# Kernel tuning notes

Measured on AMD Instinct MI355X. Metric: run time of the kernel, lower is better.

Reference implementation:

```python
import jax, jax.numpy as jnp
import numpy as np

B, SE, HD, ED, N, T = 64, 512, 1024, 512, 10000, 20
EOS_ID = 1
NEG_BIG = -1e9    # stand-in for -MAX_VAL encoder pad mask
MASK_VAL = -1e7   # logits_mask scatter value (-10000000.0 in torch)
M = HD + ED


def setup_inputs() -> dict:
    key = jax.random.key(0)
    ks = jax.random.split(key, 16)
    s = 0.02
    enc = jax.random.normal(ks[0], (B, SE, HD), jnp.float32)
    hidden = jax.random.normal(ks[1], (1, B, HD), jnp.float32)
    cell = jax.random.normal(ks[2], (1, B, HD), jnp.float32)
    text_lengths = jax.random.randint(ks[3], (B,), SE // 2, SE + 1)
    encoder_mask = jnp.arange(SE)[None, :] < text_lengths[:, None]  # [B,SE] bool
    embedding = jax.random.normal(ks[4], (N, ED), jnp.float32) * s
    # LSTM (PyTorch gate order i,f,g,o)
    w_ih = jax.random.normal(ks[5], (4 * HD, ED), jnp.float32) * s
    w_hh = jax.random.normal(ks[6], (4 * HD, HD), jnp.float32) * s
    b_ih = jnp.zeros((4 * HD,), jnp.float32)
    b_hh = jnp.zeros((4 * HD,), jnp.float32)
    # dense_net: Hd -> He
    w_q = jax.random.normal(ks[7], (HD, HD), jnp.float32) * s
    b_q = jnp.zeros((HD,), jnp.float32)
    # SelfAttentiveSum: Linear(Ed,Ed)+ReLU+Linear(Ed,1)
    w_k = jax.random.normal(ks[8], (ED, ED), jnp.float32) * s
    b_k = jnp.zeros((ED,), jnp.float32)
    w_ko = jax.random.normal(ks[9], (ED,), jnp.float32) * s
    b_ko = jnp.zeros((), jnp.float32)
    # MLP: Linear(M,M)+ReLU+Linear(M,N)
    w_m1 = jax.random.normal(ks[10], (M, M), jnp.float32) * s
    b_m1 = jnp.zeros((M,), jnp.float32)
    w_m2 = jax.random.normal(ks[11], (N, M), jnp.float32) * s
    b_m2 = jnp.zeros((N,), jnp.float32)
    return dict(encoded_hidden_embeddings=enc, hidden=hidden, cell=cell,
                text_lengths=text_lengths, encoder_mask=encoder_mask,
                embedding=embedding, w_ih=w_ih, w_hh=w_hh, b_ih=b_ih, b_hh=b_hh,
                w_q=w_q, b_q=b_q, w_k=w_k, b_k=b_k, w_ko=w_ko, b_ko=b_ko,
                w_m1=w_m1, b_m1=b_m1, w_m2=w_m2, b_m2=b_m2)


def _decode(enc, h0, c0, encoder_mask, embedding, w_ih, w_hh, b_ih, b_hh,
            w_q, b_q, w_k, b_k, w_ko, b_ko, w_m1, b_m1, w_m2, b_m2):
    pad_mask = jnp.where(encoder_mask, 0.0, NEG_BIG).astype(enc.dtype)  # [B,SE]
    sent = enc[:, 0, :]  # [B,HD] sentence representation (dropout is identity in eval)

    def step(carry, t):
        h, c, inp, logits_mask, buf = carry
        # --- LSTM cell (single step) ---
        gates = inp @ w_ih.T + b_ih + h @ w_hh.T + b_hh  # [B,4HD]
        i, f, g, o = jnp.split(gates, 4, axis=-1)
        c = jax.nn.sigmoid(f) * c + jax.nn.sigmoid(i) * jnp.tanh(g)
        h = jax.nn.sigmoid(o) * jnp.tanh(c)
        # --- attention over encoder states ---
        q = h @ w_q.T + b_q                                   # [B,HD]
        score = jnp.einsum('bsh,bh->bs', enc, q) + pad_mask    # [B,SE]
        w = jax.nn.softmax(score, axis=1)
        attn_enc = jnp.einsum('bs,bsh->bh', w, enc)            # [B,HD]
        # --- self-attentive sum over previously predicted label embeddings ---
        valid = jnp.arange(T) < jnp.maximum(t, 1)              # step 0: zeros row 0 valid
        k = jax.nn.relu(buf @ w_k.T + b_k) @ w_ko + b_ko       # [B,T]
        k = jnp.where(valid[None, :], k, NEG_BIG)
        sw = jax.nn.softmax(k, axis=1)
        attn_last = jnp.einsum('bt,bte->be', sw, buf)          # [B,ED]
        # --- MLP ---
        m = jnp.concatenate([sent + attn_enc, inp + attn_last], axis=-1)  # [B,M]
        logits = jax.nn.relu(m @ w_m1.T + b_m1) @ w_m2.T + b_m2 + logits_mask  # [B,N]
        next_ids = jnp.argmax(logits, axis=-1)                 # [B]
        pred_emb = embedding[next_ids]                          # [B,ED]
        buf = buf.at[:, t].set(pred_emb)
        logits_mask = logits_mask.at[jnp.arange(B), next_ids].set(MASK_VAL)
        logits_mask = logits_mask.at[:, EOS_ID].set(0.0)
        return (h, c, pred_emb, logits_mask, buf), (logits, next_ids)

    init = (h0, c0,
            jnp.zeros((B, ED), enc.dtype),
            jnp.zeros((B, N), enc.dtype),
            jnp.zeros((B, T, ED), enc.dtype))
    _, (outs, ids) = jax.lax.scan(step, init, jnp.arange(T))
    return jnp.transpose(outs, (1, 0, 2)), jnp.transpose(ids, (1, 0))  # [B,T,N],[B,T]


def reference(encoded_hidden_embeddings, hidden, cell, text_lengths, encoder_mask,
              embedding, w_ih, w_hh, b_ih, b_hh, w_q, b_q, w_k, b_k, w_ko, b_ko,
              w_m1, b_m1, w_m2, b_m2):
    # De=1: [1,B,HD] -> [B,HD]
    return _decode(encoded_hidden_embeddings, hidden[0], cell[0], encoder_mask,
                   embedding, w_ih, w_hh, b_ih, b_hh, w_q, b_q, w_k, b_k,
                   w_ko, b_ko, w_m1, b_m1, w_m2, b_m2)
```

## Files before the change

kernel.cpp:

```cpp
#include <hip/hip_runtime.h>

#define B64 64
#define SE 512
#define HD 1024
#define ED 512
#define NV 10000
#define TT 20
#define MM 1536
#define MASK_VALF -10000000.0f

#define OFF_XA    0
#define OFF_XB    98304
#define OFF_CT    196608
#define OFF_QF    262144
#define OFF_FM    327680
#define OFF_FL    328704
#define OFF_FACC  329728
#define OFF_XT2   1378304
#define OFF_H1T   1476608
#define OFF_ARGV  1574912
#define OFF_ARGI  1654912
#define OFF_MASKT 1734912
#define OFF_BUF   2374912
#define OFF_BUFT  3030272
#define OFF_KVP   3685632

__device__ __forceinline__ float sigmoidf_(float x) { return 1.f / (1.f + expf(-x)); }

__global__ __launch_bounds__(256) void k_init(const float* __restrict__ h0,
                                              const float* __restrict__ c0,
                                              float* __restrict__ ws) {
  int idx = blockIdx.x * 256 + threadIdx.x, stride = gridDim.x * 256;
  float* xa = ws + OFF_XA;
  float* cT = ws + OFF_CT;
  float* maskT = ws + OFF_MASKT;
  float* buf = ws + OFF_BUF;
  float* bufT = ws + OFF_BUFT;
  for (int i = idx; i < 512 * 64; i += stride) xa[i] = 0.f;
  for (int i = idx; i < NV * 64; i += stride) maskT[i] = 0.f;
  for (int i = idx; i < B64 * TT * ED; i += stride) { buf[i] = 0.f; bufT[i] = 0.f; }
  for (int i = idx; i < HD * 64; i += stride) {
    int u = i >> 6, b = i & 63;
    xa[512 * 64 + i] = h0[b * HD + u];
    cT[i] = c0[b * HD + u];
  }
}

__global__ __launch_bounds__(256) void k_cell(const float* __restrict__ xcur,
                                              const float* __restrict__ w_ih,
                                              const float* __restrict__ w_hh,
                                              const float* __restrict__ b_ih,
                                              const float* __restrict__ b_hh,
                                              float* __restrict__ cT,
                                              float* __restrict__ xnext) {
  __shared__ float wl[8 * 1536];
  int tid = threadIdx.x;
  int u0 = blockIdx.x * 2;
  for (int i = tid; i < 3072; i += 256) {
    int lr = i / 384, kq = i % 384;
    int k = kq * 4;
    int grow = (lr >> 1) * 1024 + u0 + (lr & 1);
    float4 v;
    if (k < 512) v = *(const float4*)&w_ih[(size_t)grow * 512 + k];
    else v = *(const float4*)&w_hh[(size_t)grow * 1024 + (k - 512)];
    *(float4*)&wl[lr * 1536 + k] = v;
  }
  __syncthreads();
  int lane = tid & 63, wid = tid >> 6;
  int kbase = wid * 384;
  const float* xp = xcur + (size_t)kbase * 64 + lane;
  float acc[8] = {0, 0, 0, 0, 0, 0, 0, 0};
#pragma unroll 2
  for (int k4 = 0; k4 < 96; ++k4) {
    float x0 = xp[(4 * k4 + 0) * 64];
    float x1 = xp[(4 * k4 + 1) * 64];
    float x2 = xp[(4 * k4 + 2) * 64];
    float x3 = xp[(4 * k4 + 3) * 64];
#pragma unroll
    for (int lr = 0; lr < 8; ++lr) {
      const float4 w4 = *(const float4*)&wl[lr * 1536 + kbase + 4 * k4];
      acc[lr] = fmaf(w4.x, x0, acc[lr]);
      acc[lr] = fmaf(w4.y, x1, acc[lr]);
      acc[lr] = fmaf(w4.z, x2, acc[lr]);
      acc[lr] = fmaf(w4.w, x3, acc[lr]);
    }
  }
  __syncthreads();
#pragma unroll
  for (int lr = 0; lr < 8; ++lr) wl[wid * 512 + lr * 64 + lane] = acc[lr];
  __syncthreads();
  if (tid < 128) {
    int j = tid >> 6, b = tid & 63;
    float g4[4];
#pragma unroll
    for (int g = 0; g < 4; ++g) {
      int lr = g * 2 + j;
      int grow = g * 1024 + u0 + j;
      float v = b_ih[grow] + b_hh[grow];
#pragma unroll
      for (int w = 0; w < 4; ++w) v += wl[w * 512 + lr * 64 + b];
      g4[g] = v;
    }
    int u = u0 + j;
    float c = cT[u * 64 + b];
    float cn = sigmoidf_(g4[1]) * c + sigmoidf_(g4[0]) * tanhf(g4[2]);
    float hn = sigmoidf_(g4[3]) * tanhf(cn);
    cT[u * 64 + b] = cn;
    xnext[(512 + u) * 64 + b] = hn;
  }
}

__global__ __launch_bounds__(256) void k_q2(const float* __restrict__ h,
                                            const float* __restrict__ w_q,
                                            const float* __restrict__ b_q,
                                            float* __restrict__ qf) {
  __shared__ float wl[8 * 1024];
  int tid = threadIdx.x;
  int h0 = blockIdx.x * 8;
  for (int i = tid; i < 2048; i += 256) {
    int lr = i >> 8, kq = i & 255;
    *(float4*)&wl[lr * 1024 + kq * 4] = *(const float4*)&w_q[(size_t)(h0 + lr) * 1024 + kq * 4];
  }
  __syncthreads();
  int lane = tid & 63, wid = tid >> 6;
  int kbase = wid * 256;
  const float* xp = h + (size_t)kbase * 64 + lane;
  float acc[8] = {0, 0, 0, 0, 0, 0, 0, 0};
#pragma unroll 2
  for (int k4 = 0; k4 < 64; ++k4) {
    float x0 = xp[(4 * k4 + 0) * 64];
    float x1 = xp[(4 * k4 + 1) * 64];
    float x2 = xp[(4 * k4 + 2) * 64];
    float x3 = xp[(4 * k4 + 3) * 64];
#pragma unroll
    for (int lr = 0; lr < 8; ++lr) {
      const float4 w4 = *(const float4*)&wl[lr * 1024 + kbase + 4 * k4];
      acc[lr] = fmaf(w4.x, x0, acc[lr]);
      acc[lr] = fmaf(w4.y, x1, acc[lr]);
      acc[lr] = fmaf(w4.z, x2, acc[lr]);
      acc[lr] = fmaf(w4.w, x3, acc[lr]);
    }
  }
  __syncthreads();
#pragma unroll
  for (int lr = 0; lr < 8; ++lr) wl[wid * 512 + lr * 64 + lane] = acc[lr];
  __syncthreads();
  for (int e = tid; e < 512; e += 256) {
    int lr = e >> 6, b = e & 63;
    float v = b_q[h0 + lr];
#pragma unroll
    for (int w = 0; w < 4; ++w) v += wl[w * 512 + lr * 64 + b];
    qf[(size_t)b * 1024 + h0 + lr] = v;
  }
}

__global__ __launch_bounds__(256) void k_flash(const float* __restrict__ enc,
                                               const int* __restrict__ tlen,
                                               const float* __restrict__ qf,
                                               float* __restrict__ fm, float* __restrict__ fl,
                                               float* __restrict__ facc) {
  __shared__ float lacc[4][1024];
  __shared__ float lml[4][2];
  int b = blockIdx.x >> 4, split = blockIdx.x & 15;
  int tid = threadIdx.x, lane = tid & 63, wid = tid >> 6;
  int len = tlen[b];
  float qv[16];
#pragma unroll
  for (int j = 0; j < 4; ++j) {
    float4 tq = *(const float4*)&qf[(size_t)b * 1024 + j * 256 + lane * 4];
    qv[4 * j + 0] = tq.x; qv[4 * j + 1] = tq.y; qv[4 * j + 2] = tq.z; qv[4 * j + 3] = tq.w;
  }
  const float* base = enc + (size_t)b * SE * HD;
  int s0 = split * 32 + wid * 8;
  int nr = len - s0;
  nr = nr < 0 ? 0 : (nr > 8 ? 8 : nr);
  int npair = nr >> 1;

  float4 cA[4], cB[4], nA[4], nB[4];
  float m = -1e30f, l = 0.f, acc[16];
#pragma unroll
  for (int j = 0; j < 16; ++j) acc[j] = 0.f;

#define LOADROW(d, s)                                                 \
  {                                                                   \
    const float4* rp = (const float4*)(base + (size_t)(s)*HD) + lane; \
    d[0] = rp[0]; d[1] = rp[64]; d[2] = rp[128]; d[3] = rp[192];      \
  }

  if (npair > 0) { LOADROW(cA, s0); LOADROW(cB, s0 + 1); }
  for (int p = 0; p < npair; ++p) {
    if (p + 1 < npair) {
      LOADROW(nA, s0 + 2 * p + 2);
      LOADROW(nB, s0 + 2 * p + 3);
    } else if (nr & 1) {
      LOADROW(nA, s0 + nr - 1);
    }
    float d0 = 0.f, d1 = 0.f;
#pragma unroll
    for (int j = 0; j < 4; ++j) {
      d0 = fmaf(qv[4 * j + 0], cA[j].x, d0); d1 = fmaf(qv[4 * j + 0], cB[j].x, d1);
      d0 = fmaf(qv[4 * j + 1], cA[j].y, d0); d1 = fmaf(qv[4 * j + 1], cB[j].y, d1);
      d0 = fmaf(qv[4 * j + 2], cA[j].z, d0); d1 = fmaf(qv[4 * j + 2], cB[j].z, d1);
      d0 = fmaf(qv[4 * j + 3], cA[j].w, d0); d1 = fmaf(qv[4 * j + 3], cB[j].w, d1);
    }
#pragma unroll
    for (int off = 32; off; off >>= 1) { d0 += __shfl_xor(d0, off, 64); d1 += __shfl_xor(d1, off, 64); }
    d0 = __shfl(d0, 0, 64);
    d1 = __shfl(d1, 0, 64);
    float mn = fmaxf(m, fmaxf(d0, d1));
    float sc = expf(m - mn), p0 = expf(d0 - mn), p1 = expf(d1 - mn);
    l = l * sc + p0 + p1;
#pragma unroll
    for (int j = 0; j < 4; ++j) {
      acc[4 * j + 0] = fmaf(p1, cB[j].x, fmaf(p0, cA[j].x, acc[4 * j + 0] * sc));
      acc[4 * j + 1] = fmaf(p1, cB[j].y, fmaf(p0, cA[j].y, acc[4 * j + 1] * sc));
      acc[4 * j + 2] = fmaf(p1, cB[j].z, fmaf(p0, cA[j].z, acc[4 * j + 2] * sc));
      acc[4 * j + 3] = fmaf(p1, cB[j].w, fmaf(p0, cA[j].w, acc[4 * j + 3] * sc));
    }
    m = mn;
#pragma unroll
    for (int j = 0; j < 4; ++j) { cA[j] = nA[j]; cB[j] = nB[j]; }
  }
  if (nr & 1) {
    if (npair == 0) LOADROW(cA, s0);
    float d0 = 0.f;
#pragma unroll
    for (int j = 0; j < 4; ++j) {
      d0 = fmaf(qv[4 * j + 0], cA[j].x, d0);
      d0 = fmaf(qv[4 * j + 1], cA[j].y, d0);
      d0 = fmaf(qv[4 * j + 2], cA[j].z, d0);
      d0 = fmaf(qv[4 * j + 3], cA[j].w, d0);
    }
#pragma unroll
    for (int off = 32; off; off >>= 1) d0 += __shfl_xor(d0, off, 64);
    d0 = __shfl(d0, 0, 64);
    float mn = fmaxf(m, d0);
    float sc = expf(m - mn), p0 = expf(d0 - mn);
    l = l * sc + p0;
#pragma unroll
    for (int j = 0; j < 4; ++j) {
      acc[4 * j + 0] = fmaf(p0, cA[j].x, acc[4 * j + 0] * sc);
      acc[4 * j + 1] = fmaf(p0, cA[j].y, acc[4 * j + 1] * sc);
      acc[4 * j + 2] = fmaf(p0, cA[j].z, acc[4 * j + 2] * sc);
      acc[4 * j + 3] = fmaf(p0, cA[j].w, acc[4 * j + 3] * sc);
    }
    m = mn;
  }
#undef LOADROW
#pragma unroll
  for (int j = 0; j < 4; ++j)
    *(float4*)&lacc[wid][j * 256 + lane * 4] =
        make_float4(acc[4 * j], acc[4 * j + 1], acc[4 * j + 2], acc[4 * j + 3]);
  if (lane == 0) { lml[wid][0] = m; lml[wid][1] = l; }
  __syncthreads();
  float M = fmaxf(fmaxf(lml[0][0], lml[1][0]), fmaxf(lml[2][0], lml[3][0]));
  float w0 = expf(lml[0][0] - M), w1 = expf(lml[1][0] - M);
  float w2 = expf(lml[2][0] - M), w3 = expf(lml[3][0] - M);
  float L = w0 * lml[0][1] + w1 * lml[1][1] + w2 * lml[2][1] + w3 * lml[3][1];
  int p = b * 16 + split;
  for (int h = tid; h < 1024; h += 256)
    facc[(size_t)p * 1024 + h] =
        w0 * lacc[0][h] + w1 * lacc[1][h] + w2 * lacc[2][h] + w3 * lacc[3][h];
  if (tid == 0) { fm[p] = M; fl[p] = L; }
}

__global__ __launch_bounds__(256) void k_ctx(const float* __restrict__ enc,
                                             const float* __restrict__ fm,
                                             const float* __restrict__ fl,
                                             const float* __restrict__ facc,
                                             const float* __restrict__ kvp,
                                             const float* __restrict__ b_ko,
                                             const float* __restrict__ buf,
                                             const float* __restrict__ inpT,
                                             float* __restrict__ xT2, int tv) {
  __shared__ float pw[TT];
  int b = blockIdx.x >> 2, qd = blockIdx.x & 3;
  int tid = threadIdx.x;
  if (tid < tv) {
    float s = b_ko[0];
    for (int g = 0; g < 64; ++g) s += kvp[((size_t)g * TT + tid) * 64 + b];
    pw[tid] = s;
  }
  __syncthreads();
  float mx = -1e30f;
  for (int k = 0; k < tv; ++k) mx = fmaxf(mx, pw[k]);
  float den = 0.f;
  for (int k = 0; k < tv; ++k) den += expf(pw[k] - mx);
  float invd = 1.f / den;
  __syncthreads();
  if (tid < tv) pw[tid] = expf(pw[tid] - mx) * invd;
  __syncthreads();
  float M = -1e30f;
#pragma unroll
  for (int k = 0; k < 16; ++k) M = fmaxf(M, fm[b * 16 + k]);
  float w[16];
  float L = 0.f;
#pragma unroll
  for (int k = 0; k < 16; ++k) {
    w[k] = expf(fm[b * 16 + k] - M);
    L += w[k] * fl[b * 16 + k];
  }
  float inv = 1.f / L;
  {
    int h = qd * 256 + tid;
    float s = 0.f;
#pragma unroll
    for (int k = 0; k < 16; ++k) s += w[k] * facc[(size_t)(b * 16 + k) * 1024 + h];
    xT2[h * 64 + b] = enc[(size_t)b * SE * HD + h] + s * inv;
  }
  if (tid < 128) {
    int e = qd * 128 + tid;
    float a = 0.f;
    for (int k = 0; k < tv; ++k) a += pw[k] * buf[((size_t)b * TT + k) * 512 + e];
    xT2[(1024 + e) * 64 + b] = inpT[e * 64 + b] + a;
  }
}

__global__ __launch_bounds__(256) void k_h12(const float* __restrict__ xT2,
                                             const float* __restrict__ w_m1,
                                             const float* __restrict__ b_m1,
                                             float* __restrict__ h1T) {
  __shared__ float wl[8 * 1536];
  int tid = threadIdx.x;
  int r0 = blockIdx.x * 8;
  for (int i = tid; i < 3072; i += 256) {
    int lr = i / 384, kq = i % 384;
    *(float4*)&wl[lr * 1536 + kq * 4] = *(const float4*)&w_m1[(size_t)(r0 + lr) * MM + kq * 4];
  }
  __syncthreads();
  int lane = tid & 63, wid = tid >> 6;
  int kbase = wid * 384;
  const float* xp = xT2 + (size_t)kbase * 64 + lane;
  float acc[8] = {0, 0, 0, 0, 0, 0, 0, 0};
#pragma unroll 2
  for (int k4 = 0; k4 < 96; ++k4) {
    float x0 = xp[(4 * k4 + 0) * 64];
    float x1 = xp[(4 * k4 + 1) * 64];
    float x2 = xp[(4 * k4 + 2) * 64];
    float x3 = xp[(4 * k4 + 3) * 64];
#pragma unroll
    for (int lr = 0; lr < 8; ++lr) {
      const float4 w4 = *(const float4*)&wl[lr * 1536 + kbase + 4 * k4];
      acc[lr] = fmaf(w4.x, x0, acc[lr]);
      acc[lr] = fmaf(w4.y, x1, acc[lr]);
      acc[lr] = fmaf(w4.z, x2, acc[lr]);
      acc[lr] = fmaf(w4.w, x3, acc[lr]);
    }
  }
  __syncthreads();
#pragma unroll
  for (int lr = 0; lr < 8; ++lr) wl[wid * 512 + lr * 64 + lane] = acc[lr];
  __syncthreads();
  for (int e = tid; e < 512; e += 256) {
    int lr = e >> 6, b = e & 63;
    float v = b_m1[r0 + lr];
#pragma unroll
    for (int w = 0; w < 4; ++w) v += wl[w * 512 + lr * 64 + b];
    h1T[(size_t)(r0 + lr) * 64 + b] = fmaxf(v, 0.f);
  }
}

__global__ __launch_bounds__(256) void k_glogfin2(const float* __restrict__ h1T,
                                                  const float* __restrict__ w_m2,
                                                  const float* __restrict__ b_m2,
                                                  const float* __restrict__ maskT,
                                                  float* __restrict__ argv, int* __restrict__ argi,
                                                  float* __restrict__ out, int t) {
  __shared__ float wl[8 * 1536];
  int tid = threadIdx.x;
  int r0 = blockIdx.x * 8;
  for (int i = tid; i < 3072; i += 256) {
    int lr = i / 384, kq = i % 384;
    *(float4*)&wl[lr * 1536 + kq * 4] = *(const float4*)&w_m2[(size_t)(r0 + lr) * MM + kq * 4];
  }
  __syncthreads();
  int lane = tid & 63, wid = tid >> 6;
  int kbase = wid * 384;
  const float* xp = h1T + (size_t)kbase * 64 + lane;
  float acc[8] = {0, 0, 0, 0, 0, 0, 0, 0};
#pragma unroll 2
  for (int k4 = 0; k4 < 96; ++k4) {
    float x0 = xp[(4 * k4 + 0) * 64];
    float x1 = xp[(4 * k4 + 1) * 64];
    float x2 = xp[(4 * k4 + 2) * 64];
    float x3 = xp[(4 * k4 + 3) * 64];
#pragma unroll
    for (int lr = 0; lr < 8; ++lr) {
      const float4 w4 = *(const float4*)&wl[lr * 1536 + kbase + 4 * k4];
      acc[lr] = fmaf(w4.x, x0, acc[lr]);
      acc[lr] = fmaf(w4.y, x1, acc[lr]);
      acc[lr] = fmaf(w4.z, x2, acc[lr]);
      acc[lr] = fmaf(w4.w, x3, acc[lr]);
    }
  }
  __syncthreads();
#pragma unroll
  for (int lr = 0; lr < 8; ++lr) wl[wid * 512 + lr * 64 + lane] = acc[lr];
  __syncthreads();
  for (int e = tid; e < 512; e += 256) {
    int lr = e >> 6, b = e & 63;
    int r = r0 + lr;
    float v = b_m2[r] + maskT[(size_t)r * 64 + b];
#pragma unroll
    for (int w = 0; w < 4; ++w) v += wl[w * 512 + lr * 64 + b];
    wl[2048 + lr * 64 + b] = v;
  }
  __syncthreads();
  if (tid < 64) {
    int b = tid;
    float best = -3.4e38f;
    int bi = 0;
#pragma unroll
    for (int lr = 0; lr < 8; ++lr) {
      float v = wl[2048 + lr * 64 + b];
      if (v > best) { best = v; bi = r0 + lr; }
    }
    argv[(size_t)blockIdx.x * 64 + b] = best;
    argi[(size_t)blockIdx.x * 64 + b] = bi;
  }
  for (int e = tid; e < 512; e += 256) {
    int b = e >> 3, lr = e & 7;
    out[((size_t)b * TT + t) * NV + r0 + lr] = wl[2048 + lr * 64 + b];
  }
}

__global__ __launch_bounds__(256) void k_final(const float* __restrict__ argv,
                                               const int* __restrict__ argi,
                                               const float* __restrict__ emb,
                                               float* __restrict__ maskT,
                                               float* __restrict__ xnext,
                                               float* __restrict__ buf, float* __restrict__ bufT,
                                               float* __restrict__ out_ids, int t) {
  __shared__ float sv[256];
  __shared__ int si_[256];
  __shared__ int sid;
  int b = blockIdx.x, tid = threadIdx.x;
  float best = -3.4e38f;
  int bi = 0x7fffffff;
  for (int g = tid; g < 1250; g += 256) {
    float v = argv[(size_t)g * 64 + b];
    int idx = argi[(size_t)g * 64 + b];
    if (v > best || (v == best && idx < bi)) { best = v; bi = idx; }
  }
  sv[tid] = best;
  si_[tid] = bi;
  __syncthreads();
  for (int off = 128; off; off >>= 1) {
    if (tid < off) {
      float v2 = sv[tid + off];
      int i2 = si_[tid + off];
      if (v2 > sv[tid] || (v2 == sv[tid] && i2 < si_[tid])) { sv[tid] = v2; si_[tid] = i2; }
    }
    __syncthreads();
  }
  if (tid == 0) {
    sid = si_[0];
    out_ids[b * TT + t] = (float)si_[0];
    if (si_[0] != 1) maskT[(size_t)si_[0] * 64 + b] = MASK_VALF;
  }
  __syncthreads();
  int id = sid;
  for (int e = tid; e < 512; e += 256) {
    float v = emb[(size_t)id * 512 + e];
    xnext[e * 64 + b] = v;
    buf[((size_t)b * TT + t) * 512 + e] = v;
    bufT[(size_t)e * (TT * 64) + t * 64 + b] = v;
  }
}

__global__ __launch_bounds__(256) void k_kscore(const float* __restrict__ bufT,
                                                const float* __restrict__ w_k,
                                                const float* __restrict__ b_k,
                                                const float* __restrict__ w_ko,
                                                float* __restrict__ kvp, int j) {
  __shared__ float sacc[4][8][64];
  int lane = threadIdx.x & 63, wid = threadIdx.x >> 6;
  int ug = blockIdx.x;
  int u0 = ug * 8;
  int k0 = wid * 128;
  const float* xp = bufT + (size_t)j * 64 + lane;
  float acc[8] = {0, 0, 0, 0, 0, 0, 0, 0};
  for (int k4 = 0; k4 < 32; ++k4) {
    int e = k0 + 4 * k4;
    float x0 = xp[(size_t)(e + 0) * (TT * 64)];
    float x1 = xp[(size_t)(e + 1) * (TT * 64)];
    float x2 = xp[(size_t)(e + 2) * (TT * 64)];
    float x3 = xp[(size_t)(e + 3) * (TT * 64)];
#pragma unroll
    for (int i = 0; i < 8; ++i) {
      const float4 w4 = *(const float4*)&w_k[(size_t)(u0 + i) * 512 + e];
      acc[i] = fmaf(w4.x, x0, acc[i]);
      acc[i] = fmaf(w4.y, x1, acc[i]);
      acc[i] = fmaf(w4.z, x2, acc[i]);
      acc[i] = fmaf(w4.w, x3, acc[i]);
    }
  }
#pragma unroll
  for (int i = 0; i < 8; ++i) sacc[wid][i][lane] = acc[i];
  __syncthreads();
  if (wid == 0) {
    float kp = 0.f;
#pragma unroll
    for (int i = 0; i < 8; ++i) {
      float tot = b_k[u0 + i] + sacc[0][i][lane] + sacc[1][i][lane] + sacc[2][i][lane] +
                  sacc[3][i][lane];
      kp += fmaxf(tot, 0.f) * w_ko[u0 + i];
    }
    kvp[((size_t)ug * TT + j) * 64 + lane] = kp;
  }
}

extern "C" void kernel_launch(void* const* d_in, const int* in_sizes, int n_in,
                              void* d_out, int out_size, void* d_ws, size_t ws_size,
                              hipStream_t stream) {
  const float* enc = (const float*)d_in[0];
  const float* h0 = (const float*)d_in[1];
  const float* c0 = (const float*)d_in[2];
  const int* tlen = (const int*)d_in[3];
  const float* emb = (const float*)d_in[5];
  const float* w_ih = (const float*)d_in[6];
  const float* w_hh = (const float*)d_in[7];
  const float* b_ih = (const float*)d_in[8];
  const float* b_hh = (const float*)d_in[9];
  const float* w_q = (const float*)d_in[10];
  const float* b_q = (const float*)d_in[11];
  const float* w_k = (const float*)d_in[12];
  const float* b_k = (const float*)d_in[13];
  const float* w_ko = (const float*)d_in[14];
  const float* b_ko = (const float*)d_in[15];
  const float* w_m1 = (const float*)d_in[16];
  const float* b_m1 = (const float*)d_in[17];
  const float* w_m2 = (const float*)d_in[18];
  const float* b_m2 = (const float*)d_in[19];

  float* ws = (float*)d_ws;
  float* out_logits = (float*)d_out;
  float* out_ids = out_logits + (size_t)B64 * TT * NV;

  k_init<<<2048, 256, 0, stream>>>(h0, c0, ws);
  k_kscore<<<64, 256, 0, stream>>>(ws + OFF_BUFT, w_k, b_k, w_ko, ws + OFF_KVP, 0);

  for (int t = 0; t < TT; ++t) {
    int tv = (t < 1) ? 1 : t;
    float* xcur = ws + ((t & 1) ? OFF_XB : OFF_XA);
    float* xnext = ws + ((t & 1) ? OFF_XA : OFF_XB);
    k_cell<<<512, 256, 0, stream>>>(xcur, w_ih, w_hh, b_ih, b_hh, ws + OFF_CT, xnext);
    k_q2<<<128, 256, 0, stream>>>(xnext + 512 * 64, w_q, b_q, ws + OFF_QF);
    k_flash<<<1024, 256, 0, stream>>>(enc, tlen, ws + OFF_QF, ws + OFF_FM, ws + OFF_FL,
                                      ws + OFF_FACC);
    k_ctx<<<256, 256, 0, stream>>>(enc, ws + OFF_FM, ws + OFF_FL, ws + OFF_FACC, ws + OFF_KVP,
                                   b_ko, ws + OFF_BUF, xcur, ws + OFF_XT2, tv);
    k_h12<<<192, 256, 0, stream>>>(ws + OFF_XT2, w_m1, b_m1, ws + OFF_H1T);
    k_glogfin2<<<1250, 256, 0, stream>>>(ws + OFF_H1T, w_m2, b_m2, ws + OFF_MASKT, ws + OFF_ARGV,
                                         (int*)(ws + OFF_ARGI), out_logits, t);
    k_final<<<64, 256, 0, stream>>>(ws + OFF_ARGV, (int*)(ws + OFF_ARGI), emb, ws + OFF_MASKT,
                                    xnext, ws + OFF_BUF, ws + OFF_BUFT, out_ids, t);
    if (t < TT - 1)
      k_kscore<<<64, 256, 0, stream>>>(ws + OFF_BUFT, w_k, b_k, w_ko, ws + OFF_KVP, t);
  }
}
```

Before: 3.491 ms.

## Split vocab projection into register-tiled split-K GEMM plus finalize kernel

Replaces the fused vocab-projection/argmax kernel with two kernels. The first is a 2D register-tiled GEMM (128 rows x 64 batch per block, 8x4 outputs per thread) with split-K over 6 chunks, writing partial sums to a new workspace region. The second sums the partials, adds bias and mask, computes per-group argmax, and writes the logits transposed through shared memory with float4 stores. The aim is more arithmetic per shared-memory load than the old per-row dot product. The cost is an extra launch and a round trip through global memory for the partial sums.

```diff
diff --git a/kernel.cpp b/kernel.cpp
--- a/kernel.cpp
+++ b/kernel.cpp
@@ -24,6 +24,7 @@
 #define OFF_BUF   2374912
 #define OFF_BUFT  3030272
 #define OFF_KVP   3685632
+#define OFF_LP    3767552
 
 __device__ __forceinline__ float sigmoidf_(float x) { return 1.f / (1.f + expf(-x)); }
 
@@ -360,67 +361,109 @@
   }
 }
 
-__global__ __launch_bounds__(256) void k_glogfin2(const float* __restrict__ h1T,
-                                                  const float* __restrict__ w_m2,
-                                                  const float* __restrict__ b_m2,
-                                                  const float* __restrict__ maskT,
-                                                  float* __restrict__ argv, int* __restrict__ argi,
-                                                  float* __restrict__ out, int t) {
-  __shared__ float wl[8 * 1536];
+__global__ __launch_bounds__(256) void k_vocab(const float* __restrict__ h1T,
+                                               const float* __restrict__ w_m2,
+                                               float* __restrict__ lp) {
+  __shared__ float Wl[128 * 36];
+  __shared__ float Xl[32 * 68];
   int tid = threadIdx.x;
-  int r0 = blockIdx.x * 8;
-  for (int i = tid; i < 3072; i += 256) {
-    int lr = i / 384, kq = i % 384;
-    *(float4*)&wl[lr * 1536 + kq * 4] = *(const float4*)&w_m2[(size_t)(r0 + lr) * MM + kq * 4];
-  }
-  __syncthreads();
-  int lane = tid & 63, wid = tid >> 6;
-  int kbase = wid * 384;
-  const float* xp = h1T + (size_t)kbase * 64 + lane;
-  float acc[8] = {0, 0, 0, 0, 0, 0, 0, 0};
+  int r0b = blockIdx.x * 128;
+  int k0 = blockIdx.y * 256;
+  int tc = tid & 15, tr = tid >> 4;
+  int r0 = tr * 8, b0 = tc * 4;
+  float4 acc[8];
+#pragma unroll
+  for (int i = 0; i < 8; ++i) acc[i] = make_float4(0.f, 0.f, 0.f, 0.f);
+  for (int kt = 0; kt < 8; ++kt) {
+    int kbase = k0 + kt * 32;
+#pragma unroll
+    for (int j = 0; j < 4; ++j) {
+      int f = tid + 256 * j;
+      int row = f >> 3, kkq = (f & 7) * 4;
+      int gr = r0b + row;
+      if (gr > NV - 1) gr = NV - 1;
+      *(float4*)&Wl[row * 36 + kkq] = *(const float4*)&w_m2[(size_t)gr * MM + kbase + kkq];
+    }
+#pragma unroll
+    for (int j = 0; j < 2; ++j) {
+      int f = tid + 256 * j;
+      int kk = f >> 4, bq = (f & 15) * 4;
+      *(float4*)&Xl[kk * 68 + bq] = *(const float4*)&h1T[(size_t)(kbase + kk) * 64 + bq];
+    }
+    __syncthreads();
 #pragma unroll 2
-  for (int k4 = 0; k4 < 96; ++k4) {
-    float x0 = xp[(4 * k4 + 0) * 64];
-    float x1 = xp[(4 * k4 + 1) * 64];
-    float x2 = xp[(4 * k4 + 2) * 64];
-    float x3 = xp[(4 * k4 + 3) * 64];
-#pragma unroll
-    for (int lr = 0; lr < 8; ++lr) {
-      const float4 w4 = *(const float4*)&wl[lr * 1536 + kbase + 4 * k4];
-      acc[lr] = fmaf(w4.x, x0, acc[lr]);
-      acc[lr] = fmaf(w4.y, x1, acc[lr]);
-      acc[lr] = fmaf(w4.z, x2, acc[lr]);
-      acc[lr] = fmaf(w4.w, x3, acc[lr]);
-    }
-  }
-  __syncthreads();
-#pragma unroll
-  for (int lr = 0; lr < 8; ++lr) wl[wid * 512 + lr * 64 + lane] = acc[lr];
-  __syncthreads();
-  for (int e = tid; e < 512; e += 256) {
-    int lr = e >> 6, b = e & 63;
-    int r = r0 + lr;
-    float v = b_m2[r] + maskT[(size_t)r * 64 + b];
-#pragma unroll
-    for (int w = 0; w < 4; ++w) v += wl[w * 512 + lr * 64 + b];
-    wl[2048 + lr * 64 + b] = v;
-  }
-  __syncthreads();
-  if (tid < 64) {
-    int b = tid;
+    for (int kq = 0; kq < 8; ++kq) {
+      float4 xv0 = *(const float4*)&Xl[(kq * 4 + 0) * 68 + b0];
+      float4 xv1 = *(const float4*)&Xl[(kq * 4 + 1) * 68 + b0];
+      float4 xv2 = *(const float4*)&Xl[(kq * 4 + 2) * 68 + b0];
+      float4 xv3 = *(const float4*)&Xl[(kq * 4 + 3) * 68 + b0];
+#pragma unroll
+      for (int i = 0; i < 8; ++i) {
+        float4 av = *(const float4*)&Wl[(r0 + i) * 36 + kq * 4];
+        acc[i].x = fmaf(av.x, xv0.x, acc[i].x);
+        acc[i].y = fmaf(av.x, xv0.y, acc[i].y);
+        acc[i].z = fmaf(av.x, xv0.z, acc[i].z);
+        acc[i].w = fmaf(av.x, xv0.w, acc[i].w);
+        acc[i].x = fmaf(av.y, xv1.x, acc[i].x);
+        acc[i].y = fmaf(av.y, xv1.y, acc[i].y);
+        acc[i].z = fmaf(av.y, xv1.z, acc[i].z);
+        acc[i].w = fmaf(av.y, xv1.w, acc[i].w);
+        acc[i].x = fmaf(av.z, xv2.x, acc[i].x);
+        acc[i].y = fmaf(av.z, xv2.y, acc[i].y);
+        acc[i].z = fmaf(av.z, xv2.z, acc[i].z);
+        acc[i].w = fmaf(av.z, xv2.w, acc[i].w);
+        acc[i].x = fmaf(av.w, xv3.x, acc[i].x);
+        acc[i].y = fmaf(av.w, xv3.y, acc[i].y);
+        acc[i].z = fmaf(av.w, xv3.z, acc[i].z);
+        acc[i].w = fmaf(av.w, xv3.w, acc[i].w);
+      }
+    }
+    __syncthreads();
+  }
+  float* o = lp + (size_t)blockIdx.y * 640000;
+#pragma unroll
+  for (int i = 0; i < 8; ++i) {
+    int r = r0b + r0 + i;
+    if (r < NV) *(float4*)&o[(size_t)r * 64 + b0] = acc[i];
+  }
+}
+
+__global__ __launch_bounds__(256) void k_logfin(const float* __restrict__ lp,
+                                                const float* __restrict__ b_m2,
+                                                const float* __restrict__ maskT,
+                                                float* __restrict__ argv, int* __restrict__ argi,
+                                                float* __restrict__ out, int t) {
+  __shared__ float tile[32][65];
+  int lane = threadIdx.x & 63, wid = threadIdx.x >> 6;
+  int rg = blockIdx.x * 4 + wid;
+  int nb = blockIdx.x * 32;
+  if (rg < 1250) {
+    int r0 = rg * 8;
     float best = -3.4e38f;
     int bi = 0;
 #pragma unroll
-    for (int lr = 0; lr < 8; ++lr) {
-      float v = wl[2048 + lr * 64 + b];
-      if (v > best) { best = v; bi = r0 + lr; }
-    }
-    argv[(size_t)blockIdx.x * 64 + b] = best;
-    argi[(size_t)blockIdx.x * 64 + b] = bi;
-  }
-  for (int e = tid; e < 512; e += 256) {
-    int b = e >> 3, lr = e & 7;
-    out[((size_t)b * TT + t) * NV + r0 + lr] = wl[2048 + lr * 64 + b];
+    for (int i = 0; i < 8; ++i) {
+      int r = r0 + i;
+      size_t idx = (size_t)r * 64 + lane;
+      float v = b_m2[r] + maskT[idx];
+#pragma unroll
+      for (int s = 0; s < 6; ++s) v += lp[(size_t)s * 640000 + idx];
+      tile[wid * 8 + i][lane] = v;
+      if (v > best) { best = v; bi = r; }
+    }
+    argv[(size_t)rg * 64 + lane] = best;
+    argi[(size_t)rg * 64 + lane] = bi;
+  }
+  __syncthreads();
+  int b = threadIdx.x >> 2, q = threadIdx.x & 3;
+  int nloc = q * 8;
+  if (nb + nloc < NV) {
+    float tmp[8];
+#pragma unroll
+    for (int c = 0; c < 8; ++c) tmp[c] = tile[nloc + c][b];
+    float4* o = (float4*)&out[((size_t)b * TT + t) * NV + nb + nloc];
+    o[0] = make_float4(tmp[0], tmp[1], tmp[2], tmp[3]);
+    o[1] = make_float4(tmp[4], tmp[5], tmp[6], tmp[7]);
   }
 }
 
@@ -551,8 +594,9 @@
     k_ctx<<<256, 256, 0, stream>>>(enc, ws + OFF_FM, ws + OFF_FL, ws + OFF_FACC, ws + OFF_KVP,
                                    b_ko, ws + OFF_BUF, xcur, ws + OFF_XT2, tv);
     k_h12<<<192, 256, 0, stream>>>(ws + OFF_XT2, w_m1, b_m1, ws + OFF_H1T);
-    k_glogfin2<<<1250, 256, 0, stream>>>(ws + OFF_H1T, w_m2, b_m2, ws + OFF_MASKT, ws + OFF_ARGV,
-                                         (int*)(ws + OFF_ARGI), out_logits, t);
+    k_vocab<<<dim3(79, 6), 256, 0, stream>>>(ws + OFF_H1T, w_m2, ws + OFF_LP);
+    k_logfin<<<313, 256, 0, stream>>>(ws + OFF_LP, b_m2, ws + OFF_MASKT, ws + OFF_ARGV,
+                                      (int*)(ws + OFF_ARGI), out_logits, t);
     k_final<<<64, 256, 0, stream>>>(ws + OFF_ARGV, (int*)(ws + OFF_ARGI), emb, ws + OFF_MASKT,
                                     xnext, ws + OFF_BUF, ws + OFF_BUFT, out_ids, t);
     if (t < TT - 1)
```

Result: faster. 3.178 ms (-9.0%).
